# Optimization experiments

Measured on AMD Instinct MI355X. Metric: run time of the kernel, lower is better.

## Reference

```python
import jax, jax.numpy as jnp
import numpy as np

NUM_NODES = 200000
NUM_GRAPHS = 1024
D_FEAT = 512


def setup_inputs() -> dict:
    key = jax.random.key(0)
    k_x, k_j = jax.random.split(key)
    inputs = jax.random.normal(k_x, (NUM_NODES, D_FEAT), dtype=jnp.float32)
    # Contiguous, strictly-increasing segment start offsets with idx[0] == 0.
    # Base offsets split nodes ~evenly; jitter in [0, step) keeps strict monotonicity.
    step = NUM_NODES // NUM_GRAPHS  # 195
    base = (jnp.arange(NUM_GRAPHS, dtype=jnp.int32) * NUM_NODES) // NUM_GRAPHS
    jitter = jax.random.randint(k_j, (NUM_GRAPHS,), 0, step, dtype=jnp.int32)
    idx = base + jitter
    idx = idx.at[0].set(0)
    return {"inputs": inputs, "idx": idx, "num_nodes": NUM_NODES, "num_graphs": NUM_GRAPHS}


def reference(inputs, idx, num_nodes, num_graphs):
    # Original: dense [num_graphs, num_nodes] pooling matrix with row i holding
    # 1/(idx[i+1]-idx[i]) over columns idx[i]:idx[i+1], then matmul + relu.
    # Equivalent math: per-contiguous-segment mean of node features, then relu.
    node_ids = jnp.arange(num_nodes, dtype=jnp.int32)
    # segment id of node n: largest i with idx[i] <= n (idx[0]=0 -> seg >= 0)
    seg = jnp.searchsorted(idx, node_ids, side="right") - 1  # [num_nodes]
    sums = jax.ops.segment_sum(inputs, seg, num_segments=num_graphs)  # [G, D]
    idx_aug = jnp.append(idx, jnp.int32(num_nodes))
    counts = (idx_aug[1:] - idx_aug[:-1]).astype(inputs.dtype)  # [G]
    out = sums / counts[:, None]
    return jax.nn.relu(out)
```

## Files before the change

kernel.cpp:

```cpp
#include <hip/hip_runtime.h>


#define D_FEAT 512
#define NCOL4 (D_FEAT / 4)
#define MAX_SUB 4

typedef float f4 __attribute__((ext_vector_type(4)));

__global__ __launch_bounds__(512) void seg_accum_ws(
    const f4* __restrict__ in,
    const int* __restrict__ idx,
    float* __restrict__ ws,
    int num_nodes, int num_graphs, int rpb) {
  const int b = blockIdx.x;
  const int r0 = b * rpb;
  if (r0 >= num_nodes) return;
  const int r1 = min(r0 + rpb, num_nodes);

  const int lane = threadIdx.x & 63;
  const int w = threadIdx.x >> 6;

  __shared__ f4 part[8][NCOL4];

  int lo = 0, hi = num_graphs - 1;
  while (lo < hi) {
    int mid = (lo + hi + 1) >> 1;
    if (idx[mid] <= r0) lo = mid;
    else hi = mid - 1;
  }
  int s = lo;
  int row = r0;
  int k = 0;

  while (row < r1 && k < MAX_SUB) {
    const int seg_end = (s + 1 < num_graphs) ? idx[s + 1] : num_nodes;
    const int e = min(seg_end, r1);
    const int n = e - row;

    const int wsr = row + (n * w) / 8;
    const int wer = row + (n * (w + 1)) / 8;

    f4 accA = {0.f, 0.f, 0.f, 0.f};
    f4 accB = {0.f, 0.f, 0.f, 0.f};

    int j = wsr * NCOL4 + lane;
    const int jend = wer * NCOL4;
    for (; j + 192 < jend; j += 256) {
      f4 v0 = __builtin_nontemporal_load(&in[j]);
      f4 v1 = __builtin_nontemporal_load(&in[j + 64]);
      f4 v2 = __builtin_nontemporal_load(&in[j + 128]);
      f4 v3 = __builtin_nontemporal_load(&in[j + 192]);
      accA += v0;
      accB += v1;
      accA += v2;
      accB += v3;
    }
    for (; j < jend; j += 64) {
      f4 v = __builtin_nontemporal_load(&in[j]);
      if ((((j - lane) >> 6) & 1) == 0) accA += v;
      else accB += v;
    }

    part[w][lane] = accA;
    part[w][lane + 64] = accB;
    __syncthreads();

    if (threadIdx.x < NCOL4) {
      f4 a = part[0][threadIdx.x];
#pragma unroll
      for (int ww = 1; ww < 8; ++ww) a += part[ww][threadIdx.x];
      ((f4*)ws)[((size_t)b * MAX_SUB + k) * NCOL4 + threadIdx.x] = a;
    }
    __syncthreads();

    row = e;
    ++s;
    ++k;
  }
}

__global__ __launch_bounds__(512) void seg_gather(
    const float* __restrict__ ws, const int* __restrict__ idx,
    float* __restrict__ out, int num_nodes, int num_graphs, int rpb) {
  const int s = blockIdx.x;
  if (s >= num_graphs) return;
  const int t = threadIdx.x;
  const int start = idx[s];
  const int end = (s + 1 < num_graphs) ? idx[s + 1] : num_nodes;
  const int b0 = start / rpb;
  const int b1 = (end - 1) / rpb;

  float sum = 0.f;
  for (int bb = b0; bb <= b1; ++bb) {
    const int rr = bb * rpb;
    int lo = 0, hi = num_graphs - 1;
    while (lo < hi) {
      int mid = (lo + hi + 1) >> 1;
      if (idx[mid] <= rr) lo = mid;
      else hi = mid - 1;
    }
    const int local = s - lo;
    if (local >= 0 && local < MAX_SUB)
      sum += ws[((size_t)bb * MAX_SUB + local) * D_FEAT + t];
  }
  out[(size_t)s * D_FEAT + t] = fmaxf(sum / (float)(end - start), 0.f);
}

extern "C" void kernel_launch(void* const* d_in, const int* in_sizes, int n_in,
                              void* d_out, int out_size, void* d_ws,
                              size_t ws_size, hipStream_t stream) {
  const f4* in = (const f4*)d_in[0];
  const int* idx = (const int*)d_in[1];
  float* out = (float*)d_out;
  float* ws = (float*)d_ws;

  const int num_nodes = in_sizes[0] / D_FEAT;
  const int num_graphs = in_sizes[1];

  const int nblocks = 1024;
  const int rpb = (num_nodes + nblocks - 1) / nblocks;

  seg_accum_ws<<<dim3(nblocks), dim3(512), 0, stream>>>(in, idx, ws, num_nodes,
                                                        num_graphs, rpb);
  seg_gather<<<dim3(num_graphs), dim3(512), 0, stream>>>(ws, idx, out,
                                                         num_nodes, num_graphs,
                                                         rpb);
}
```

Baseline: 78.52 us.

## Fuse segment accumulate and gather via atomics with last-block finalize

Removes the separate gather kernel and the per-block sub-segment workspace. Each block now atomically adds its partial sums into a per-segment accumulator. A per-segment counter lets the last contributing block apply the mean and ReLU and write the output. The main load loop is also unrolled from 4 to 8 vector loads per iteration. In exchange, the buffers must be cleared with a memset every call, float atomics make the summation order nondeterministic, and the last-block read of the accumulator depends on correct memory ordering.

```diff
diff --git a/kernel.cpp b/kernel.cpp
--- a/kernel.cpp
+++ b/kernel.cpp
@@ -3,14 +3,15 @@
 
 #define D_FEAT 512
 #define NCOL4 (D_FEAT / 4)
-#define MAX_SUB 4
 
 typedef float f4 __attribute__((ext_vector_type(4)));
 
-__global__ __launch_bounds__(512) void seg_accum_ws(
+__global__ __launch_bounds__(512) void seg_pool_fused(
     const f4* __restrict__ in,
     const int* __restrict__ idx,
-    float* __restrict__ ws,
+    float* __restrict__ acc,
+    int* __restrict__ cnt,
+    float* __restrict__ out,
     int num_nodes, int num_graphs, int rpb) {
   const int b = blockIdx.x;
   const int r0 = b * rpb;
@@ -19,8 +20,10 @@
 
   const int lane = threadIdx.x & 63;
   const int w = threadIdx.x >> 6;
+  const int t = threadIdx.x;
 
   __shared__ f4 part[8][NCOL4];
+  __shared__ int done;
 
   int lo = 0, hi = num_graphs - 1;
   while (lo < hi) {
@@ -30,9 +33,8 @@
   }
   int s = lo;
   int row = r0;
-  int k = 0;
 
-  while (row < r1 && k < MAX_SUB) {
+  while (row < r1) {
     const int seg_end = (s + 1 < num_graphs) ? idx[s + 1] : num_nodes;
     const int e = min(seg_end, r1);
     const int n = e - row;
@@ -45,15 +47,17 @@
 
     int j = wsr * NCOL4 + lane;
     const int jend = wer * NCOL4;
-    for (; j + 192 < jend; j += 256) {
+    for (; j + 448 < jend; j += 512) {
       f4 v0 = __builtin_nontemporal_load(&in[j]);
       f4 v1 = __builtin_nontemporal_load(&in[j + 64]);
       f4 v2 = __builtin_nontemporal_load(&in[j + 128]);
       f4 v3 = __builtin_nontemporal_load(&in[j + 192]);
-      accA += v0;
-      accB += v1;
-      accA += v2;
-      accB += v3;
+      f4 v4 = __builtin_nontemporal_load(&in[j + 256]);
+      f4 v5 = __builtin_nontemporal_load(&in[j + 320]);
+      f4 v6 = __builtin_nontemporal_load(&in[j + 384]);
+      f4 v7 = __builtin_nontemporal_load(&in[j + 448]);
+      accA += v0; accB += v1; accA += v2; accB += v3;
+      accA += v4; accB += v5; accA += v6; accB += v7;
     }
     for (; j < jend; j += 64) {
       f4 v = __builtin_nontemporal_load(&in[j]);
@@ -65,45 +69,37 @@
     part[w][lane + 64] = accB;
     __syncthreads();
 
-    if (threadIdx.x < NCOL4) {
-      f4 a = part[0][threadIdx.x];
+    if (t < NCOL4) {
+      f4 a = part[0][t];
 #pragma unroll
-      for (int ww = 1; ww < 8; ++ww) a += part[ww][threadIdx.x];
-      ((f4*)ws)[((size_t)b * MAX_SUB + k) * NCOL4 + threadIdx.x] = a;
+      for (int ww = 1; ww < 8; ++ww) a += part[ww][t];
+      float* o = acc + (size_t)s * D_FEAT + t * 4;
+      atomicAdd(o + 0, a.x);
+      atomicAdd(o + 1, a.y);
+      atomicAdd(o + 2, a.z);
+      atomicAdd(o + 3, a.w);
     }
     __syncthreads();
 
+    const int seg_start = idx[s];
+    const int needed = (seg_end - 1) / rpb - seg_start / rpb + 1;
+    if (t == 0) {
+      int old = __hip_atomic_fetch_add(&cnt[s], 1, __ATOMIC_ACQ_REL,
+                                       __HIP_MEMORY_SCOPE_AGENT);
+      done = (old == needed - 1);
+    }
+    __syncthreads();
+
+    if (done) {
+      const float inv = 1.0f / (float)(seg_end - seg_start);
+      float v = __hip_atomic_load(&acc[(size_t)s * D_FEAT + t],
+                                  __ATOMIC_RELAXED, __HIP_MEMORY_SCOPE_AGENT);
+      out[(size_t)s * D_FEAT + t] = fmaxf(v * inv, 0.f);
+    }
+
     row = e;
     ++s;
-    ++k;
   }
-}
-
-__global__ __launch_bounds__(512) void seg_gather(
-    const float* __restrict__ ws, const int* __restrict__ idx,
-    float* __restrict__ out, int num_nodes, int num_graphs, int rpb) {
-  const int s = blockIdx.x;
-  if (s >= num_graphs) return;
-  const int t = threadIdx.x;
-  const int start = idx[s];
-  const int end = (s + 1 < num_graphs) ? idx[s + 1] : num_nodes;
-  const int b0 = start / rpb;
-  const int b1 = (end - 1) / rpb;
-
-  float sum = 0.f;
-  for (int bb = b0; bb <= b1; ++bb) {
-    const int rr = bb * rpb;
-    int lo = 0, hi = num_graphs - 1;
-    while (lo < hi) {
-      int mid = (lo + hi + 1) >> 1;
-      if (idx[mid] <= rr) lo = mid;
-      else hi = mid - 1;
-    }
-    const int local = s - lo;
-    if (local >= 0 && local < MAX_SUB)
-      sum += ws[((size_t)bb * MAX_SUB + local) * D_FEAT + t];
-  }
-  out[(size_t)s * D_FEAT + t] = fmaxf(sum / (float)(end - start), 0.f);
 }
 
 extern "C" void kernel_launch(void* const* d_in, const int* in_sizes, int n_in,
@@ -112,17 +108,19 @@
   const f4* in = (const f4*)d_in[0];
   const int* idx = (const int*)d_in[1];
   float* out = (float*)d_out;
-  float* ws = (float*)d_ws;
 
   const int num_nodes = in_sizes[0] / D_FEAT;
   const int num_graphs = in_sizes[1];
 
+  float* acc = (float*)d_ws;
+  int* cnt = (int*)((char*)d_ws + (size_t)num_graphs * D_FEAT * sizeof(float));
+  const size_t zero_bytes =
+      (size_t)num_graphs * D_FEAT * sizeof(float) + num_graphs * sizeof(int);
+  hipMemsetAsync(d_ws, 0, zero_bytes, stream);
+
   const int nblocks = 1024;
   const int rpb = (num_nodes + nblocks - 1) / nblocks;
 
-  seg_accum_ws<<<dim3(nblocks), dim3(512), 0, stream>>>(in, idx, ws, num_nodes,
-                                                        num_graphs, rpb);
-  seg_gather<<<dim3(num_graphs), dim3(512), 0, stream>>>(ws, idx, out,
-                                                         num_nodes, num_graphs,
-                                                         rpb);
+  seg_pool_fused<<<dim3(nblocks), dim3(512), 0, stream>>>(
+      in, idx, acc, cnt, out, num_nodes, num_graphs, rpb);
 }
```

Result: slower. 180.0 us (+129.3%).

## Split rows across 4096 blocks with single-pass predicated multi-segment accumulation

Applied to the files above, without the earlier changes.

Raises the block count to 4096, giving each block about 49 rows. Each block now streams its whole row range once, with the work split evenly across waves, and routes every loaded vector into one of three segment accumulators by comparing it against the boundary offsets. This replaces the old per-segment loop, which ran a separate pass and barrier for each segment and left waves imbalanced on short segments. The first 1920 blocks also use plain cached loads instead of nontemporal loads, presumably to keep part of the input resident in cache across runs. The cost is more accumulator registers, three select-adds per load, a larger workspace, and an assumption that no block spans more than three segments.

```diff
diff --git a/kernel.cpp b/kernel.cpp
--- a/kernel.cpp
+++ b/kernel.cpp
@@ -3,9 +3,21 @@
 
 #define D_FEAT 512
 #define NCOL4 (D_FEAT / 4)
-#define MAX_SUB 4
+#define NBLK 4096
+#define BSPLIT 1920
 
 typedef float f4 __attribute__((ext_vector_type(4)));
+
+__device__ __forceinline__ int find_seg(const int* __restrict__ idx, int G,
+                                        int r) {
+  int lo = 0, hi = G - 1;
+  while (lo < hi) {
+    int mid = (lo + hi + 1) >> 1;
+    if (idx[mid] <= r) lo = mid;
+    else hi = mid - 1;
+  }
+  return lo;
+}
 
 __global__ __launch_bounds__(512) void seg_accum_ws(
     const f4* __restrict__ in,
@@ -19,63 +31,89 @@
 
   const int lane = threadIdx.x & 63;
   const int w = threadIdx.x >> 6;
+  const int t = threadIdx.x;
 
   __shared__ f4 part[8][NCOL4];
 
-  int lo = 0, hi = num_graphs - 1;
-  while (lo < hi) {
-    int mid = (lo + hi + 1) >> 1;
-    if (idx[mid] <= r0) lo = mid;
-    else hi = mid - 1;
+  const int s0 = find_seg(idx, num_graphs, r0);
+  const int e1 = (s0 + 1 < num_graphs) ? idx[s0 + 1] : num_nodes;
+  const int e2 = (s0 + 2 < num_graphs) ? idx[s0 + 2] : num_nodes;
+  const int B1 = min(e1, r1) * NCOL4;
+  const int B2 = min(e2, r1) * NCOL4;
+
+  const int n = r1 - r0;
+  const int u0 = (2 * n * w) >> 3;
+  const int u1 = (2 * n * (w + 1)) >> 3;
+  const int js = r0 * NCOL4 + u0 * 64;
+  const int nb = u1 - u0;
+
+  const int cE = lane ^ ((u0 & 1) << 6);
+  const int cO = cE ^ 64;
+
+  f4 z = {0.f, 0.f, 0.f, 0.f};
+  f4 aE0 = z, aE1 = z, aE2 = z, aO0 = z, aO1 = z, aO2 = z;
+
+#define ACC3(v, jb, a0, a1, a2)            \
+  {                                        \
+    bool x1 = (jb) >= B1, x2 = (jb) >= B2; \
+    a0 += x1 ? z : (v);                    \
+    a1 += (x1 && !x2) ? (v) : z;           \
+    a2 += x2 ? (v) : z;                    \
   }
-  int s = lo;
-  int row = r0;
-  int k = 0;
 
-  while (row < r1 && k < MAX_SUB) {
-    const int seg_end = (s + 1 < num_graphs) ? idx[s + 1] : num_nodes;
-    const int e = min(seg_end, r1);
-    const int n = e - row;
+#define STREAM(LD)                                        \
+  {                                                       \
+    int k = 0;                                            \
+    for (; k + 4 <= nb; k += 4) {                         \
+      const int jb = js + k * 64;                         \
+      const f4* p = in + jb + lane;                       \
+      f4 v0 = LD(p);                                      \
+      f4 v1 = LD(p + 64);                                 \
+      f4 v2 = LD(p + 128);                                \
+      f4 v3 = LD(p + 192);                                \
+      ACC3(v0, jb, aE0, aE1, aE2);                        \
+      ACC3(v1, jb + 64, aO0, aO1, aO2);                   \
+      ACC3(v2, jb + 128, aE0, aE1, aE2);                  \
+      ACC3(v3, jb + 192, aO0, aO1, aO2);                  \
+    }                                                     \
+    for (; k < nb; ++k) {                                 \
+      const int jb = js + k * 64;                         \
+      f4 v = LD((in + jb + lane));                        \
+      if ((k & 1) == 0) ACC3(v, jb, aE0, aE1, aE2)        \
+      else ACC3(v, jb, aO0, aO1, aO2)                     \
+    }                                                     \
+  }
 
-    const int wsr = row + (n * w) / 8;
-    const int wer = row + (n * (w + 1)) / 8;
+#define LD_PLAIN(p) (*(p))
+#define LD_NT(p) (__builtin_nontemporal_load(p))
 
-    f4 accA = {0.f, 0.f, 0.f, 0.f};
-    f4 accB = {0.f, 0.f, 0.f, 0.f};
+  if (b < BSPLIT) {
+    STREAM(LD_PLAIN)
+  } else {
+    STREAM(LD_NT)
+  }
 
-    int j = wsr * NCOL4 + lane;
-    const int jend = wer * NCOL4;
-    for (; j + 192 < jend; j += 256) {
-      f4 v0 = __builtin_nontemporal_load(&in[j]);
-      f4 v1 = __builtin_nontemporal_load(&in[j + 64]);
-      f4 v2 = __builtin_nontemporal_load(&in[j + 128]);
-      f4 v3 = __builtin_nontemporal_load(&in[j + 192]);
-      accA += v0;
-      accB += v1;
-      accA += v2;
-      accB += v3;
-    }
-    for (; j < jend; j += 64) {
-      f4 v = __builtin_nontemporal_load(&in[j]);
-      if ((((j - lane) >> 6) & 1) == 0) accA += v;
-      else accB += v;
-    }
+#define ROUND(K, aE, aO)                                  \
+  {                                                       \
+    part[w][cE] = aE;                                     \
+    part[w][cO] = aO;                                     \
+    __syncthreads();                                      \
+    if (t < NCOL4) {                                      \
+      f4 a = part[0][t];                                  \
+      _Pragma("unroll") for (int ww = 1; ww < 8; ++ww)    \
+          a += part[ww][t];                               \
+      ((f4*)ws)[((size_t)b * 3 + K) * NCOL4 + t] = a;     \
+    }                                                     \
+  }
 
-    part[w][lane] = accA;
-    part[w][lane + 64] = accB;
+  ROUND(0, aE0, aO0)
+  if (e1 < r1) {
     __syncthreads();
-
-    if (threadIdx.x < NCOL4) {
-      f4 a = part[0][threadIdx.x];
-#pragma unroll
-      for (int ww = 1; ww < 8; ++ww) a += part[ww][threadIdx.x];
-      ((f4*)ws)[((size_t)b * MAX_SUB + k) * NCOL4 + threadIdx.x] = a;
-    }
+    ROUND(1, aE1, aO1)
+  }
+  if (e2 < r1) {
     __syncthreads();
-
-    row = e;
-    ++s;
-    ++k;
+    ROUND(2, aE2, aO2)
   }
 }
 
@@ -92,16 +130,8 @@
 
   float sum = 0.f;
   for (int bb = b0; bb <= b1; ++bb) {
-    const int rr = bb * rpb;
-    int lo = 0, hi = num_graphs - 1;
-    while (lo < hi) {
-      int mid = (lo + hi + 1) >> 1;
-      if (idx[mid] <= rr) lo = mid;
-      else hi = mid - 1;
-    }
-    const int local = s - lo;
-    if (local >= 0 && local < MAX_SUB)
-      sum += ws[((size_t)bb * MAX_SUB + local) * D_FEAT + t];
+    const int c = s - find_seg(idx, num_graphs, bb * rpb);
+    if (c >= 0 && c < 3) sum += ws[((size_t)bb * 3 + c) * D_FEAT + t];
   }
   out[(size_t)s * D_FEAT + t] = fmaxf(sum / (float)(end - start), 0.f);
 }
@@ -117,11 +147,10 @@
   const int num_nodes = in_sizes[0] / D_FEAT;
   const int num_graphs = in_sizes[1];
 
-  const int nblocks = 1024;
-  const int rpb = (num_nodes + nblocks - 1) / nblocks;
+  const int rpb = (num_nodes + NBLK - 1) / NBLK;
 
-  seg_accum_ws<<<dim3(nblocks), dim3(512), 0, stream>>>(in, idx, ws, num_nodes,
-                                                        num_graphs, rpb);
+  seg_accum_ws<<<dim3(NBLK), dim3(512), 0, stream>>>(in, idx, ws, num_nodes,
+                                                     num_graphs, rpb);
   seg_gather<<<dim3(num_graphs), dim3(512), 0, stream>>>(ws, idx, out,
                                                          num_nodes, num_graphs,
                                                          rpb);
```

Result: slower. 91.33 us (+16.3%).
